# Kernel optimization log

Measured on AMD Instinct MI355X. Metric: run time of the kernel, lower is better.

The kernel has to match this reference:

```python
import jax, jax.numpy as jnp
import numpy as np

# (dy, dx) offsets corresponding to the single -1 entries of kernels 1..8
# delta1 rows: (0,0),(0,1),(0,2),(1,2); delta2 = spatial flip: (2,2),(2,1),(2,0),(1,0)
OFFSETS = [(-1, -1), (-1, 0), (-1, 1), (0, 1), (1, 1), (1, 0), (1, -1), (0, -1)]
NUM_LAYER = 9
EPS = 1e-12


def _shift(x, dy, dx):
    # zero-padded shift: out[y, x] = in[y + dy, x + dx]; dilation = shifts[0] = 1
    b, c, h, w = x.shape
    p = jnp.pad(x, ((0, 0), (0, 0), (1, 1), (1, 1)))
    return jax.lax.dynamic_slice(p, (0, 0, 1 + dy, 1 + dx), (b, c, h, w))


def _l2norm(v, axis):
    # matches torch.nn.functional.normalize: v / max(||v||, eps)
    n = jnp.sqrt(jnp.sum(v * v, axis=axis, keepdims=True))
    return v / jnp.maximum(n, EPS)


def setup_inputs() -> dict:
    key = jax.random.key(0)
    k1, k2, k3, k4 = jax.random.split(key, 4)
    B, C, H, W = 4, 256, 96, 96
    cen = jax.random.normal(k1, (B, C, H, W), dtype=jnp.float32)
    scale = 1.0 / np.sqrt(C)
    # grouped 1x1 convs (groups=9): per-group (C x C) weight matrices
    W1 = jax.random.normal(k2, (NUM_LAYER, C, C), dtype=jnp.float32) * scale
    W2 = jax.random.normal(k3, (C, C), dtype=jnp.float32) * scale
    W3 = jax.random.normal(k4, (NUM_LAYER, C, C), dtype=jnp.float32) * scale
    return {"cen": cen, "W1": W1, "W2": W2, "W3": W3}


def reference(cen, W1, W2, W3):
    b, c, h, w = cen.shape
    # Extract_layer: 8 fixed depthwise 3x3 convs (each = negated shift) + identity
    surrounds = jnp.stack(
        [-_shift(cen, dy, dx) for dy, dx in OFFSETS] + [cen], axis=1
    )  # (b, 9, c, h, w)
    # Analyze_layer: grouped 1x1 convs = per-group matmuls
    out1 = jnp.einsum("gij,bgjhw->bgihw", W1, surrounds)
    out2 = jnp.einsum("ij,bjhw->bihw", W2, cen)[:, None]  # (b, 1, c, h, w)
    out3 = jnp.einsum("gij,bgjhw->bgihw", W3, surrounds)
    out1 = _l2norm(out1, axis=2)
    out2 = _l2norm(out2, axis=2)
    out3 = _l2norm(out3, axis=2)
    # softmax over a size-1 axis (dim=2 after mean+keepdim) -> identically 1.0
    att = jax.nn.softmax(
        jnp.mean(out1 * out2, axis=2, keepdims=True), axis=2
    )  # (b, 9, 1, h, w)
    out = jnp.sum(att * out3, axis=1)  # (b, c, h, w)
    return out + cen
```

## Files before the change

kernel.cpp:

```cpp
#include <hip/hip_runtime.h>
#include <stdint.h>

#define BB 4
#define CC 256
#define HH 96
#define WW 96
#define HP 98
#define CP 264
#define XT 32
#define YT 2
#define XE 34

typedef __bf16 bf16x8 __attribute__((ext_vector_type(8)));
typedef float f32x4 __attribute__((ext_vector_type(4)));
typedef float f32x16 __attribute__((ext_vector_type(16)));
typedef uint32_t u32x4 __attribute__((ext_vector_type(4)));

__device__ __forceinline__ uint16_t f2bf(float f) {
    uint32_t u = __float_as_uint(f);
    u += 0x7FFFu + ((u >> 16) & 1u);
    return (uint16_t)(u >> 16);
}

__global__ void zero_halo(uint16_t* __restrict__ cenT) {
    int idx = blockIdx.x * 256 + threadIdx.x;
    if (idx >= 1552 * 33) return;
    int p = idx / 33, q = idx - p * 33;
    int b = p / 388, s = p - b * 388;
    int y, x;
    if (s < 98)      { y = 0;       x = s; }
    else if (s < 196){ y = 97;      x = s - 98; }
    else if (s < 292){ x = 0;       y = s - 196 + 1; }
    else             { x = 97;      y = s - 292 + 1; }
    size_t o = (((size_t)b * HP + y) * HP + x) * CP + q * 8;
    *(uint4*)(cenT + o) = make_uint4(0u, 0u, 0u, 0u);
}

__global__ void transpose_cen(const float* __restrict__ cen, uint16_t* __restrict__ cenT) {
    const int y = blockIdx.x, b = blockIdx.y, ch = blockIdx.z, tid = threadIdx.x;
    __shared__ uint16_t ldsX[128 * 100];

    #pragma unroll
    for (int i = 0; i < 12; ++i) {
        int f = i * 256 + tid;
        int c = f / 24, xq = f % 24;
        float4 v = *(const float4*)(cen + ((((size_t)b * CC + ch * 128 + c) * HH + y) * WW + xq * 4));
        uint2 pk;
        pk.x = (uint32_t)f2bf(v.x) | ((uint32_t)f2bf(v.y) << 16);
        pk.y = (uint32_t)f2bf(v.z) | ((uint32_t)f2bf(v.w) << 16);
        *(uint2*)(&ldsX[c * 100 + xq * 4]) = pk;
    }
    __syncthreads();
    #pragma unroll
    for (int i = 0; i < 6; ++i) {
        int t = i * 256 + tid;
        int x = t % 96, cq = t / 96;
        uint32_t w0, w1, w2, w3;
        w0 = (uint32_t)ldsX[(cq * 8 + 0) * 100 + x] | ((uint32_t)ldsX[(cq * 8 + 1) * 100 + x] << 16);
        w1 = (uint32_t)ldsX[(cq * 8 + 2) * 100 + x] | ((uint32_t)ldsX[(cq * 8 + 3) * 100 + x] << 16);
        w2 = (uint32_t)ldsX[(cq * 8 + 4) * 100 + x] | ((uint32_t)ldsX[(cq * 8 + 5) * 100 + x] << 16);
        w3 = (uint32_t)ldsX[(cq * 8 + 6) * 100 + x] | ((uint32_t)ldsX[(cq * 8 + 7) * 100 + x] << 16);
        size_t o = (((size_t)b * HP + (y + 1)) * HP + (x + 1)) * CP + ch * 128 + cq * 8;
        *(uint4*)(cenT + o) = make_uint4(w0, w1, w2, w3);
    }
}

__global__ void cvt_w3(const float* __restrict__ W3, uint16_t* __restrict__ W3bf) {
    int e = (blockIdx.x * 256 + threadIdx.x) * 4;
    int g = e >> 16, n = (e >> 8) & 255, k = e & 255;
    float4 v = *(const float4*)(W3 + e);
    uint2 pk;
    pk.x = (uint32_t)f2bf(v.x) | ((uint32_t)f2bf(v.y) << 16);
    pk.y = (uint32_t)f2bf(v.z) | ((uint32_t)f2bf(v.w) << 16);
    size_t o = (size_t)(((g * 8 + (n >> 5)) * 16 + (k >> 4)) * 512)
             + (n & 31) * 16 + ((k >> 3) & 1) * 8 + (k & 7);
    *(uint2*)(W3bf + o) = pk;
}

__global__ __launch_bounds__(256, 2)
void ecm_main(const float* __restrict__ cen, const uint16_t* __restrict__ cenT,
              const uint16_t* __restrict__ W3bf, float* __restrict__ out) {
    const int tid = threadIdx.x;
    const int wv = tid >> 6, lane = tid & 63, col = lane & 31, kh = lane >> 5;
    const int x0 = blockIdx.x * XT, y0 = blockIdx.y * YT, b = blockIdx.z;

    __shared__ __align__(16) uint16_t ldsA[YT * XE * CP];
    __shared__ __align__(16) float ldsP[2][64][4];

    const int dgOrd[9] = {0, 1, 2, 7, 8, 3, 6, 5, 4};

    const uint16_t* wbA = W3bf + (size_t)(2 * wv) * (16 * 512) + col * 16 + kh * 8;
    f32x16 finA0 = {}, finA1 = {}, finB0 = {}, finB1 = {};

    #pragma unroll 1
    for (int idx = 0; idx < 9; ++idx) {
        const int g = dgOrd[idx], dg = idx / 3, dx = idx % 3 - 1;

        if (idx % 3 == 0) {
            for (int r = 0; r < YT; ++r) {
                const u32x4* gs = (const u32x4*)(cenT + (((size_t)b * HP + (y0 + dg + r)) * HP + x0) * CP);
                u32x4* ls = (u32x4*)(ldsA + r * XE * CP);
                for (int c = tid; c < XE * CP / 8; c += 256) {
                    u32x4 v = __builtin_nontemporal_load(gs + c);
                    ls[c] = v;
                }
            }
            __syncthreads();
        }

        const uint16_t* wgA = wbA + (size_t)g * 65536;
        const uint16_t* wgB = wgA + 16 * 512;
        const int a0 = (col + dx + 1) * CP + kh * 8;
        const int a1 = a0 + XE * CP;

        f32x16 aA0 = {}, aA1 = {}, aB0 = {}, aB1 = {};

        bf16x8 qA[2], qB[2];
        qA[0] = *(const bf16x8*)(wgA);
        qB[0] = *(const bf16x8*)(wgB);
        qA[1] = *(const bf16x8*)(wgA + 512);
        qB[1] = *(const bf16x8*)(wgB + 512);
        bf16x8 b0 = *(const bf16x8*)(ldsA + a0);
        bf16x8 b1 = *(const bf16x8*)(ldsA + a1);

        #pragma unroll
        for (int ks = 0; ks < 16; ++ks) {
            bf16x8 wa = qA[ks & 1], wb = qB[ks & 1];
            if (ks + 2 < 16) {
                qA[ks & 1] = *(const bf16x8*)(wgA + (ks + 2) * 512);
                qB[ks & 1] = *(const bf16x8*)(wgB + (ks + 2) * 512);
            }
            bf16x8 n0 = b0, n1 = b1;
            if (ks + 1 < 16) {
                n0 = *(const bf16x8*)(ldsA + a0 + (ks + 1) * 16);
                n1 = *(const bf16x8*)(ldsA + a1 + (ks + 1) * 16);
            }
            aA0 = __builtin_amdgcn_mfma_f32_32x32x16_bf16(wa, b0, aA0, 0, 0, 0);
            aB0 = __builtin_amdgcn_mfma_f32_32x32x16_bf16(wb, b0, aB0, 0, 0, 0);
            aA1 = __builtin_amdgcn_mfma_f32_32x32x16_bf16(wa, b1, aA1, 0, 0, 0);
            aB1 = __builtin_amdgcn_mfma_f32_32x32x16_bf16(wb, b1, aB1, 0, 0, 0);
            b0 = n0; b1 = n1;
        }

        float s0 = 0.f, s1 = 0.f;
        #pragma unroll
        for (int r = 0; r < 16; ++r) {
            s0 += aA0[r] * aA0[r] + aB0[r] * aB0[r];
            s1 += aA1[r] * aA1[r] + aB1[r] * aB1[r];
        }
        s0 += __shfl_xor(s0, 32, 64);
        s1 += __shfl_xor(s1, 32, 64);
        if (kh == 0) { ldsP[idx & 1][col][wv] = s0; ldsP[idx & 1][32 + col][wv] = s1; }
        __syncthreads();

        f32x4 pa = *(const f32x4*)&ldsP[idx & 1][col][0];
        f32x4 qa = *(const f32x4*)&ldsP[idx & 1][32 + col][0];
        float n0 = pa[0] + pa[1] + pa[2] + pa[3];
        float n1 = qa[0] + qa[1] + qa[2] + qa[3];
        const float sgn = (g == 8) ? 1.f : -1.f;
        float sc0 = sgn / fmaxf(sqrtf(n0), 1e-12f);
        float sc1 = sgn / fmaxf(sqrtf(n1), 1e-12f);
        #pragma unroll
        for (int r = 0; r < 16; ++r) {
            finA0[r] += aA0[r] * sc0; finB0[r] += aB0[r] * sc0;
            finA1[r] += aA1[r] * sc1; finB1[r] += aB1[r] * sc1;
        }
    }

    #pragma unroll
    for (int r = 0; r < 16; ++r) {
        int chA = wv * 64 + (r & 3) + 8 * (r >> 2) + 4 * kh;
        size_t oA0 = (((size_t)b * CC + chA) * HH + y0) * WW + (x0 + col);
        size_t oA1 = oA0 + WW;
        __builtin_nontemporal_store(finA0[r] + __builtin_nontemporal_load(cen + oA0), out + oA0);
        __builtin_nontemporal_store(finA1[r] + __builtin_nontemporal_load(cen + oA1), out + oA1);
        size_t oB0 = oA0 + (size_t)32 * HH * WW;
        size_t oB1 = oB0 + WW;
        __builtin_nontemporal_store(finB0[r] + __builtin_nontemporal_load(cen + oB0), out + oB0);
        __builtin_nontemporal_store(finB1[r] + __builtin_nontemporal_load(cen + oB1), out + oB1);
    }
}

extern "C" void kernel_launch(void* const* d_in, const int* in_sizes, int n_in,
                              void* d_out, int out_size, void* d_ws, size_t ws_size,
                              hipStream_t stream) {
    const float* cen = (const float*)d_in[0];
    const float* W3 = (const float*)d_in[3];
    float* out = (float*)d_out;

    uint16_t* cenT = (uint16_t*)d_ws;
    const size_t cenT_elems = (size_t)BB * HP * HP * CP;
    uint16_t* W3bf = cenT + cenT_elems;

    zero_halo<<<201, 256, 0, stream>>>(cenT);
    transpose_cen<<<dim3(HH, BB, 2), 256, 0, stream>>>(cen, cenT);
    cvt_w3<<<576, 256, 0, stream>>>(W3, W3bf);
    ecm_main<<<dim3(3, 48, 4), 256, 0, stream>>>(cen, cenT, W3bf, out);
}
```

Baseline: 193.4 us.

## Store final accumulators in bf16, deepen weight prefetch, set MFMA priority

The four final output accumulators are now held as bf16 vectors instead of f32, roughly halving the registers they occupy, which could help occupancy. Weight fragments are prefetched four k-steps ahead instead of two. MFMA issue is wrapped in s_setprio raise/lower. Nontemporal loads and stores are replaced with plain ones. Summing the nine groups in bf16 loses accuracy and, together with the extra prefetch registers, may change register allocation in ways that are hard to predict.

```diff
diff --git a/kernel.cpp b/kernel.cpp
--- a/kernel.cpp
+++ b/kernel.cpp
@@ -12,9 +12,9 @@
 #define XE 34
 
 typedef __bf16 bf16x8 __attribute__((ext_vector_type(8)));
+typedef __bf16 bf16x16 __attribute__((ext_vector_type(16)));
 typedef float f32x4 __attribute__((ext_vector_type(4)));
 typedef float f32x16 __attribute__((ext_vector_type(16)));
-typedef uint32_t u32x4 __attribute__((ext_vector_type(4)));
 
 __device__ __forceinline__ uint16_t f2bf(float f) {
     uint32_t u = __float_as_uint(f);
@@ -90,7 +90,7 @@
     const int dgOrd[9] = {0, 1, 2, 7, 8, 3, 6, 5, 4};
 
     const uint16_t* wbA = W3bf + (size_t)(2 * wv) * (16 * 512) + col * 16 + kh * 8;
-    f32x16 finA0 = {}, finA1 = {}, finB0 = {}, finB1 = {};
+    bf16x16 finA0 = {}, finA1 = {}, finB0 = {}, finB1 = {};
 
     #pragma unroll 1
     for (int idx = 0; idx < 9; ++idx) {
@@ -98,12 +98,9 @@
 
         if (idx % 3 == 0) {
             for (int r = 0; r < YT; ++r) {
-                const u32x4* gs = (const u32x4*)(cenT + (((size_t)b * HP + (y0 + dg + r)) * HP + x0) * CP);
-                u32x4* ls = (u32x4*)(ldsA + r * XE * CP);
-                for (int c = tid; c < XE * CP / 8; c += 256) {
-                    u32x4 v = __builtin_nontemporal_load(gs + c);
-                    ls[c] = v;
-                }
+                const uint4* gs = (const uint4*)(cenT + (((size_t)b * HP + (y0 + dg + r)) * HP + x0) * CP);
+                uint4* ls = (uint4*)(ldsA + r * XE * CP);
+                for (int c = tid; c < XE * CP / 8; c += 256) ls[c] = gs[c];
             }
             __syncthreads();
         }
@@ -115,30 +112,33 @@
 
         f32x16 aA0 = {}, aA1 = {}, aB0 = {}, aB1 = {};
 
-        bf16x8 qA[2], qB[2];
-        qA[0] = *(const bf16x8*)(wgA);
-        qB[0] = *(const bf16x8*)(wgB);
-        qA[1] = *(const bf16x8*)(wgA + 512);
-        qB[1] = *(const bf16x8*)(wgB + 512);
+        bf16x8 qA[4], qB[4];
+        #pragma unroll
+        for (int i = 0; i < 4; ++i) {
+            qA[i] = *(const bf16x8*)(wgA + i * 512);
+            qB[i] = *(const bf16x8*)(wgB + i * 512);
+        }
         bf16x8 b0 = *(const bf16x8*)(ldsA + a0);
         bf16x8 b1 = *(const bf16x8*)(ldsA + a1);
 
         #pragma unroll
         for (int ks = 0; ks < 16; ++ks) {
-            bf16x8 wa = qA[ks & 1], wb = qB[ks & 1];
-            if (ks + 2 < 16) {
-                qA[ks & 1] = *(const bf16x8*)(wgA + (ks + 2) * 512);
-                qB[ks & 1] = *(const bf16x8*)(wgB + (ks + 2) * 512);
+            bf16x8 wa = qA[ks & 3], wb = qB[ks & 3];
+            if (ks + 4 < 16) {
+                qA[ks & 3] = *(const bf16x8*)(wgA + (ks + 4) * 512);
+                qB[ks & 3] = *(const bf16x8*)(wgB + (ks + 4) * 512);
             }
             bf16x8 n0 = b0, n1 = b1;
             if (ks + 1 < 16) {
                 n0 = *(const bf16x8*)(ldsA + a0 + (ks + 1) * 16);
                 n1 = *(const bf16x8*)(ldsA + a1 + (ks + 1) * 16);
             }
+            __builtin_amdgcn_s_setprio(1);
             aA0 = __builtin_amdgcn_mfma_f32_32x32x16_bf16(wa, b0, aA0, 0, 0, 0);
             aB0 = __builtin_amdgcn_mfma_f32_32x32x16_bf16(wb, b0, aB0, 0, 0, 0);
             aA1 = __builtin_amdgcn_mfma_f32_32x32x16_bf16(wa, b1, aA1, 0, 0, 0);
             aB1 = __builtin_amdgcn_mfma_f32_32x32x16_bf16(wb, b1, aB1, 0, 0, 0);
+            __builtin_amdgcn_s_setprio(0);
             b0 = n0; b1 = n1;
         }
 
@@ -162,8 +162,10 @@
         float sc1 = sgn / fmaxf(sqrtf(n1), 1e-12f);
         #pragma unroll
         for (int r = 0; r < 16; ++r) {
-            finA0[r] += aA0[r] * sc0; finB0[r] += aB0[r] * sc0;
-            finA1[r] += aA1[r] * sc1; finB1[r] += aB1[r] * sc1;
+            finA0[r] = (__bf16)((float)finA0[r] + aA0[r] * sc0);
+            finB0[r] = (__bf16)((float)finB0[r] + aB0[r] * sc0);
+            finA1[r] = (__bf16)((float)finA1[r] + aA1[r] * sc1);
+            finB1[r] = (__bf16)((float)finB1[r] + aB1[r] * sc1);
         }
     }
 
@@ -172,12 +174,12 @@
         int chA = wv * 64 + (r & 3) + 8 * (r >> 2) + 4 * kh;
         size_t oA0 = (((size_t)b * CC + chA) * HH + y0) * WW + (x0 + col);
         size_t oA1 = oA0 + WW;
-        __builtin_nontemporal_store(finA0[r] + __builtin_nontemporal_load(cen + oA0), out + oA0);
-        __builtin_nontemporal_store(finA1[r] + __builtin_nontemporal_load(cen + oA1), out + oA1);
+        out[oA0] = (float)finA0[r] + cen[oA0];
+        out[oA1] = (float)finA1[r] + cen[oA1];
         size_t oB0 = oA0 + (size_t)32 * HH * WW;
         size_t oB1 = oB0 + WW;
-        __builtin_nontemporal_store(finB0[r] + __builtin_nontemporal_load(cen + oB0), out + oB0);
-        __builtin_nontemporal_store(finB1[r] + __builtin_nontemporal_load(cen + oB1), out + oB1);
+        out[oB0] = (float)finB0[r] + cen[oB0];
+        out[oB1] = (float)finB1[r] + cen[oB1];
     }
 }
 
```

Result: faster. 171.6 us (-11.3%).
